# Optimization experiments

Hardware: AMD Instinct MI355X
Metric: run time of the kernel (lower is better)

Reference implementation:

```python
import jax, jax.numpy as jnp
import numpy as np

# ActivationWithGain: activation scaled so a standard-normal input keeps unit variance.
_s = np.random.default_rng(0).standard_normal(1 << 20).astype(np.float32)
GAIN = float(1.0 / (_s / (1.0 + np.exp(-_s))).std())  # SiLU gain ~ 1.787
INV_SQRT2 = np.float32(1.0 / np.sqrt(2.0))


def _act(x):
    return jax.nn.silu(x) * jnp.float32(GAIN)


def setup_inputs() -> dict:
    key = jax.random.key(0)
    ks = jax.random.split(key, 9)
    n_up, n_dn, n_nuc, dim, edim = 512, 512, 256, 256, 32
    n_el = n_up + n_dn
    n_edges = n_el * n_nuc  # dense electron-nucleus bipartite graph
    return {
        "elec_emb": jax.random.normal(ks[0], (n_el, dim), jnp.float32),
        "up_inp": jax.random.normal(ks[1], (n_nuc, dim), jnp.float32),
        "down_inp": jax.random.normal(ks[2], (n_nuc, dim), jnp.float32),
        "edge_emb": jax.random.normal(ks[3], (n_edges, edim), jnp.float32),
        "contr": jax.random.uniform(ks[4], (n_edges,), jnp.float32),
        "norm": jax.random.uniform(ks[5], (n_el,), jnp.float32),
        "W_out": jax.random.normal(ks[6], (dim, dim), jnp.float32) / np.float32(np.sqrt(dim)),
        "b_out": jnp.zeros((dim,), jnp.float32),
        "W_edge": jax.random.normal(ks[7], (edim, dim), jnp.float32) / np.float32(np.sqrt(edim)),
        "W_out2": jax.random.normal(ks[8], (dim, dim), jnp.float32) / np.float32(np.sqrt(dim)),
        "b_out2": jnp.zeros((dim,), jnp.float32),
        "scale1": jnp.ones((), jnp.float32),  # FixedScalingFactor (frozen after init)
        "scale2": jnp.ones((), jnp.float32),
        "n_up": n_up,
        "n_down": n_dn,
        "n_nuclei": n_nuc,
    }


def reference(elec_emb, up_inp, down_inp, edge_emb, contr, norm,
              W_out, b_out, W_edge, W_out2, b_out2, scale1, scale2,
              n_up, n_down, n_nuclei):
    n_el = n_up + n_down
    # adj_idx for a single graph: dense bipartite edges, sorted by electron index
    e_n_i = jnp.repeat(jnp.arange(n_el), n_nuclei)   # [E] electron index per edge
    e_n_k = jnp.tile(jnp.arange(n_nuclei), n_el)     # [E] nucleus index per edge

    out_emb = elec_emb @ W_out + b_out               # Dense(out_dim)

    mask = jnp.arange(n_el) < n_up                   # spin_mask: True for spin-up electrons
    e_n_mask = mask[e_n_i]
    # gather nuclear embeddings per edge, selecting up/down table by electron spin
    inp = jnp.where(e_n_mask[:, None], up_inp[e_n_k], down_inp[e_n_k])  # [E, D]

    weights = edge_emb @ W_edge                      # Dense_no_bias(out_dim), [E, D]
    # FixedScalingFactor: contr only weights the init-time variance estimate;
    # at runtime the op is x * scale1.
    to_elec = inp * weights * scale1                 # [E, D]

    agg = jax.ops.segment_sum(to_elec, e_n_i, num_segments=n_el,
                              indices_are_sorted=True)  # [n_el, D]
    out_emb = (out_emb + agg * norm[:, None]) * scale2
    out_emb = _act(out_emb)
    out_emb = _act(out_emb @ W_out2 + b_out2)
    # residual: shapes match, so rescaled sum
    return (elec_emb + out_emb) * INV_SQRT2
```

## Files before the change

kernel.cpp:

```cpp
#include <hip/hip_runtime.h>
#include <hip/hip_bf16.h>

#define N_EL   1024
#define N_UP   512
#define NNUC   256
#define DIM    256
#define EDIM   32

#define GAIN_F      1.7872135f
#define INV_SQRT2_F 0.7071067811865476f

typedef __attribute__((ext_vector_type(8))) short bf16x8;
typedef __attribute__((ext_vector_type(4))) short bf16x4;
typedef __attribute__((ext_vector_type(4))) float f32x4;

__device__ __forceinline__ short f2bf(float x) {
    union { __hip_bfloat16 h; short s; } u;
    u.h = __float2bfloat16(x);
    return u.s;
}

__global__ __launch_bounds__(256) void prep_kernel(
    const float* __restrict__ up, const float* __restrict__ dn,
    const float* __restrict__ wedge,
    const float* __restrict__ w1, const float* __restrict__ w2,
    const float* __restrict__ elec,
    float* __restrict__ tab_up, float* __restrict__ tab_dn,
    short* __restrict__ wedge_arr,
    short* __restrict__ w1f, short* __restrict__ w2f,
    short* __restrict__ elecb)
{
    const int idx = (blockIdx.x << 8) + threadIdx.x;

    {
        const int kt = idx >> 12;
        const int dt = (idx >> 8) & 15;
        const int l  = (idx >> 2) & 63;
        const int r  = idx & 3;
        const int row = (kt << 4) + ((l >> 4) << 2) + r;
        const int col = (dt << 4) + (l & 15);
        tab_up[idx] = up[row * DIM + col];
        tab_dn[idx] = dn[row * DIM + col];
    }
    if (idx < 16 * 64 * 8) {
        const int dt2 = idx >> 9;
        const int l2  = (idx >> 3) & 63;
        const int b   = idx & 7;
        const int j   = ((l2 >> 4) << 3) + b;
        const int d   = (dt2 << 4) + (l2 & 15);
        wedge_arr[idx] = f2bf(wedge[j * DIM + d]);
    }
    {
        const int b  = idx & 7;
        const int l  = (idx >> 3) & 63;
        const int q  = (idx >> 9) & 7;
        const int nt = idx >> 12;
        const int j  = (q << 5) + ((l >> 4) << 3) + b;
        const int d  = (nt << 4) + (l & 15);
        w1f[idx] = f2bf(w1[j * DIM + d]);
        w2f[idx] = f2bf(w2[j * DIM + d]);
    }
    {
        const f32x4 v = *(const f32x4*)(elec + (idx << 2));
        bf16x4 o;
        o[0] = f2bf(v[0]); o[1] = f2bf(v[1]); o[2] = f2bf(v[2]); o[3] = f2bf(v[3]);
        *(bf16x4*)(elecb + (idx << 2)) = o;
    }
}

__global__ __launch_bounds__(256) void fused_kernel(
    const float* __restrict__ eemb,
    const float* __restrict__ tab_up, const float* __restrict__ tab_dn,
    const short* __restrict__ wedge_arr,
    const short* __restrict__ w1f, const short* __restrict__ w2f,
    const short* __restrict__ elecb, const float* __restrict__ elec,
    const float* __restrict__ norm,
    const float* __restrict__ b1, const float* __restrict__ b2,
    const float* __restrict__ s1p, const float* __restrict__ s2p,
    float* __restrict__ outp)
{
    __shared__ float part[4][4][256];
    __shared__ float agg_s[4][256];
    __shared__ short h_s[4][256];

    const int tid  = threadIdx.x;
    const int bid  = blockIdx.x;
    const int w    = tid >> 6;
    const int lane = tid & 63;
    const int g    = lane >> 4;
    const int c    = lane & 15;
    const int base = bid << 2;

    {
        const float* __restrict__ tab = (base < N_UP) ? tab_up : tab_dn;

        bf16x8 a[4][4];
        #pragma unroll
        for (int e = 0; e < 4; ++e) {
            #pragma unroll
            for (int q = 0; q < 4; ++q) {
                const int kt = (w << 2) + q;
                const float* src = eemb +
                    ((size_t)((base + e) * NNUC + (kt << 4) + c) * EDIM + (g << 3));
                f32x4 lo = *(const f32x4*)(src);
                f32x4 hi = *(const f32x4*)(src + 4);
                union { bf16x8 v; short s[8]; } f;
                f.s[0] = f2bf(lo[0]); f.s[1] = f2bf(lo[1]);
                f.s[2] = f2bf(lo[2]); f.s[3] = f2bf(lo[3]);
                f.s[4] = f2bf(hi[0]); f.s[5] = f2bf(hi[1]);
                f.s[6] = f2bf(hi[2]); f.s[7] = f2bf(hi[3]);
                a[e][q] = f.v;
            }
        }

        const int kt0 = (w << 2);
        bf16x8 bnxt = *(const bf16x8*)(wedge_arr + (lane << 3));
        f32x4 tn0, tn1, tn2, tn3;
        tn0 = *(const f32x4*)(tab + ((((kt0 + 0) << 4) + 0) * 64 + lane) * 4);
        tn1 = *(const f32x4*)(tab + ((((kt0 + 1) << 4) + 0) * 64 + lane) * 4);
        tn2 = *(const f32x4*)(tab + ((((kt0 + 2) << 4) + 0) * 64 + lane) * 4);
        tn3 = *(const f32x4*)(tab + ((((kt0 + 3) << 4) + 0) * 64 + lane) * 4);

        const f32x4 zero4 = {0.f, 0.f, 0.f, 0.f};

        #pragma unroll 1
        for (int dt = 0; dt < 16; ++dt) {
            const bf16x8 bcur = bnxt;
            const f32x4 t0 = tn0, t1 = tn1, t2 = tn2, t3 = tn3;
            if (dt < 15) {
                bnxt = *(const bf16x8*)(wedge_arr + (((dt + 1) << 6) + lane) * 8);
                tn0 = *(const f32x4*)(tab + ((((kt0 + 0) << 4) + dt + 1) * 64 + lane) * 4);
                tn1 = *(const f32x4*)(tab + ((((kt0 + 1) << 4) + dt + 1) * 64 + lane) * 4);
                tn2 = *(const f32x4*)(tab + ((((kt0 + 2) << 4) + dt + 1) * 64 + lane) * 4);
                tn3 = *(const f32x4*)(tab + ((((kt0 + 3) << 4) + dt + 1) * 64 + lane) * 4);
            }
            float p[4] = {0.f, 0.f, 0.f, 0.f};
            #pragma unroll
            for (int e = 0; e < 4; ++e) {
                f32x4 cc;
                cc = __builtin_amdgcn_mfma_f32_16x16x32_bf16(a[e][0], bcur, zero4, 0, 0, 0);
                p[e] += cc[0] * t0[0] + cc[1] * t0[1] + cc[2] * t0[2] + cc[3] * t0[3];
                cc = __builtin_amdgcn_mfma_f32_16x16x32_bf16(a[e][1], bcur, zero4, 0, 0, 0);
                p[e] += cc[0] * t1[0] + cc[1] * t1[1] + cc[2] * t1[2] + cc[3] * t1[3];
                cc = __builtin_amdgcn_mfma_f32_16x16x32_bf16(a[e][2], bcur, zero4, 0, 0, 0);
                p[e] += cc[0] * t2[0] + cc[1] * t2[1] + cc[2] * t2[2] + cc[3] * t2[3];
                cc = __builtin_amdgcn_mfma_f32_16x16x32_bf16(a[e][3], bcur, zero4, 0, 0, 0);
                p[e] += cc[0] * t3[0] + cc[1] * t3[1] + cc[2] * t3[2] + cc[3] * t3[3];
            }
            #pragma unroll
            for (int e = 0; e < 4; ++e) {
                float v = p[e];
                v += __shfl_xor(v, 16, 64);
                v += __shfl_xor(v, 32, 64);
                if (lane < 16) part[w][e][(dt << 4) + lane] = v;
            }
        }
    }
    __syncthreads();
    {
        const float s1 = *s1p;
        for (int t = tid; t < 4 * 256; t += 256) {
            const int e = t >> 8;
            const int d = t & 255;
            agg_s[e][d] = (part[0][e][d] + part[1][e][d] +
                           part[2][e][d] + part[3][e][d]) * s1;
        }
    }
    __syncthreads();

    {
        const float s2 = *s2p;
        const int arow = (base + c) & (N_EL - 1);
        const short* abase = elecb + (arow << 8) + (g << 3);

        bf16x8 a[8];
        #pragma unroll
        for (int q = 0; q < 8; ++q) a[q] = *(const bf16x8*)(abase + (q << 5));

        const short* bb0 = w1f + ((w << 2) << 12) + (lane << 3);
        bf16x8 b[8], bn[8];
        #pragma unroll
        for (int q = 0; q < 8; ++q) bn[q] = *(const bf16x8*)(bb0 + (q << 9));

        #pragma unroll
        for (int t = 0; t < 4; ++t) {
            #pragma unroll
            for (int q = 0; q < 8; ++q) b[q] = bn[q];
            if (t < 3) {
                const short* bbn = bb0 + ((t + 1) << 12);
                #pragma unroll
                for (int q = 0; q < 8; ++q) bn[q] = *(const bf16x8*)(bbn + (q << 9));
            }
            f32x4 acc = {0.f, 0.f, 0.f, 0.f};
            #pragma unroll
            for (int q = 0; q < 8; ++q)
                acc = __builtin_amdgcn_mfma_f32_16x16x32_bf16(a[q], b[q], acc, 0, 0, 0);

            if (g == 0) {
                const int nt = (w << 2) + t;
                const int n  = (nt << 4) + c;
                const float bv = b1[n];
                #pragma unroll
                for (int r = 0; r < 4; ++r) {
                    const float y = (acc[r] + bv + agg_s[r][n] * norm[base + r]) * s2;
                    const float sig = 1.f / (1.f + __expf(-y));
                    h_s[r][n] = f2bf(GAIN_F * y * sig);
                }
            }
        }
    }
    __syncthreads();

    {
        bf16x8 a[8];
        #pragma unroll
        for (int q = 0; q < 8; ++q)
            a[q] = *(const bf16x8*)(&h_s[c & 3][(q << 5) + (g << 3)]);

        const short* bb0 = w2f + ((w << 2) << 12) + (lane << 3);
        bf16x8 b[8], bn[8];
        #pragma unroll
        for (int q = 0; q < 8; ++q) bn[q] = *(const bf16x8*)(bb0 + (q << 9));

        #pragma unroll
        for (int t = 0; t < 4; ++t) {
            #pragma unroll
            for (int q = 0; q < 8; ++q) b[q] = bn[q];
            if (t < 3) {
                const short* bbn = bb0 + ((t + 1) << 12);
                #pragma unroll
                for (int q = 0; q < 8; ++q) bn[q] = *(const bf16x8*)(bbn + (q << 9));
            }
            f32x4 acc = {0.f, 0.f, 0.f, 0.f};
            #pragma unroll
            for (int q = 0; q < 8; ++q)
                acc = __builtin_amdgcn_mfma_f32_16x16x32_bf16(a[q], b[q], acc, 0, 0, 0);

            if (g == 0) {
                const int nt = (w << 2) + t;
                const int n  = (nt << 4) + c;
                const float bv = b2[n];
                #pragma unroll
                for (int r = 0; r < 4; ++r) {
                    const float z = acc[r] + bv;
                    const float sig = 1.f / (1.f + __expf(-z));
                    const float o = GAIN_F * z * sig;
                    const int m = base + r;
                    outp[(m << 8) + n] = (elec[(m << 8) + n] + o) * INV_SQRT2_F;
                }
            }
        }
    }
}

extern "C" void kernel_launch(void* const* d_in, const int* in_sizes, int n_in,
                              void* d_out, int out_size, void* d_ws, size_t ws_size,
                              hipStream_t stream)
{
    const float* elec  = (const float*)d_in[0];
    const float* up    = (const float*)d_in[1];
    const float* dn    = (const float*)d_in[2];
    const float* eemb  = (const float*)d_in[3];
    const float* norm  = (const float*)d_in[5];
    const float* W1    = (const float*)d_in[6];
    const float* b1    = (const float*)d_in[7];
    const float* Wedge = (const float*)d_in[8];
    const float* W2    = (const float*)d_in[9];
    const float* b2    = (const float*)d_in[10];
    const float* s1    = (const float*)d_in[11];
    const float* s2    = (const float*)d_in[12];

    float* ws     = (float*)d_ws;
    float* tab_up = ws;
    float* tab_dn = ws + 65536;
    short* sbase  = (short*)(ws + 131072);
    short* warr   = sbase;
    short* w1f    = sbase + 8192;
    short* w2f    = sbase + 8192 + 65536;
    short* elecb  = sbase + 8192 + 131072;

    prep_kernel <<<256, 256, 0, stream>>>(up, dn, Wedge, W1, W2, elec,
                                          tab_up, tab_dn, warr, w1f, w2f, elecb);
    fused_kernel<<<256, 256, 0, stream>>>(eemb, tab_up, tab_dn, warr, w1f, w2f,
                                          elecb, elec, norm, b1, b2, s1, s2,
                                          (float*)d_out);
}
```

Baseline: 34.43 us.

## Split fused kernel into edge aggregation and separate 16-row output MLP kernel

Splits the single fused kernel into an edge kernel, which writes the aggregated per-electron vectors to a global workspace, and a separate output kernel. The output kernel runs both dense layers on 16-row tiles, so each MFMA uses all 16 rows. The old fused version padded 4 real rows to 16, which wasted most of the MFMA work and re-read the weight matrices in every one of 256 blocks. The cost is an extra kernel launch, a round trip through global memory for the aggregate, and only 64 blocks in the output stage.

After: 36.24 us. +5.3%, slower.

```diff
diff --git a/kernel.cpp b/kernel.cpp
--- a/kernel.cpp
+++ b/kernel.cpp
@@ -68,187 +68,171 @@
     }
 }
 
-__global__ __launch_bounds__(256) void fused_kernel(
+__global__ __launch_bounds__(256) void edge_kernel(
     const float* __restrict__ eemb,
     const float* __restrict__ tab_up, const float* __restrict__ tab_dn,
     const short* __restrict__ wedge_arr,
-    const short* __restrict__ w1f, const short* __restrict__ w2f,
-    const short* __restrict__ elecb, const float* __restrict__ elec,
-    const float* __restrict__ norm,
-    const float* __restrict__ b1, const float* __restrict__ b2,
-    const float* __restrict__ s1p, const float* __restrict__ s2p,
-    float* __restrict__ outp)
+    const float* __restrict__ s1p,
+    float* __restrict__ agg)
 {
     __shared__ float part[4][4][256];
-    __shared__ float agg_s[4][256];
-    __shared__ short h_s[4][256];
-
     const int tid  = threadIdx.x;
-    const int bid  = blockIdx.x;
     const int w    = tid >> 6;
     const int lane = tid & 63;
     const int g    = lane >> 4;
     const int c    = lane & 15;
-    const int base = bid << 2;
-
-    {
-        const float* __restrict__ tab = (base < N_UP) ? tab_up : tab_dn;
-
-        bf16x8 a[4][4];
+    const int base = blockIdx.x << 2;
+    const float* __restrict__ tab = (base < N_UP) ? tab_up : tab_dn;
+
+    bf16x8 a[4][4];
+    #pragma unroll
+    for (int e = 0; e < 4; ++e) {
+        #pragma unroll
+        for (int q = 0; q < 4; ++q) {
+            const int kt = (w << 2) + q;
+            const float* src = eemb +
+                ((size_t)((base + e) * NNUC + (kt << 4) + c) * EDIM + (g << 3));
+            f32x4 lo = *(const f32x4*)(src);
+            f32x4 hi = *(const f32x4*)(src + 4);
+            union { bf16x8 v; short s[8]; } f;
+            f.s[0] = f2bf(lo[0]); f.s[1] = f2bf(lo[1]);
+            f.s[2] = f2bf(lo[2]); f.s[3] = f2bf(lo[3]);
+            f.s[4] = f2bf(hi[0]); f.s[5] = f2bf(hi[1]);
+            f.s[6] = f2bf(hi[2]); f.s[7] = f2bf(hi[3]);
+            a[e][q] = f.v;
+        }
+    }
+
+    const int kt0 = (w << 2);
+    bf16x8 bnxt = *(const bf16x8*)(wedge_arr + (lane << 3));
+    f32x4 tn0, tn1, tn2, tn3;
+    tn0 = *(const f32x4*)(tab + ((((kt0 + 0) << 4) + 0) * 64 + lane) * 4);
+    tn1 = *(const f32x4*)(tab + ((((kt0 + 1) << 4) + 0) * 64 + lane) * 4);
+    tn2 = *(const f32x4*)(tab + ((((kt0 + 2) << 4) + 0) * 64 + lane) * 4);
+    tn3 = *(const f32x4*)(tab + ((((kt0 + 3) << 4) + 0) * 64 + lane) * 4);
+
+    const f32x4 zero4 = {0.f, 0.f, 0.f, 0.f};
+
+    #pragma unroll 1
+    for (int dt = 0; dt < 16; ++dt) {
+        const bf16x8 bcur = bnxt;
+        const f32x4 t0 = tn0, t1 = tn1, t2 = tn2, t3 = tn3;
+        if (dt < 15) {
+            bnxt = *(const bf16x8*)(wedge_arr + (((dt + 1) << 6) + lane) * 8);
+            tn0 = *(const f32x4*)(tab + ((((kt0 + 0) << 4) + dt + 1) * 64 + lane) * 4);
+            tn1 = *(const f32x4*)(tab + ((((kt0 + 1) << 4) + dt + 1) * 64 + lane) * 4);
+            tn2 = *(const f32x4*)(tab + ((((kt0 + 2) << 4) + dt + 1) * 64 + lane) * 4);
+            tn3 = *(const f32x4*)(tab + ((((kt0 + 3) << 4) + dt + 1) * 64 + lane) * 4);
+        }
+        float p[4] = {0.f, 0.f, 0.f, 0.f};
         #pragma unroll
         for (int e = 0; e < 4; ++e) {
-            #pragma unroll
-            for (int q = 0; q < 4; ++q) {
-                const int kt = (w << 2) + q;
-                const float* src = eemb +
-                    ((size_t)((base + e) * NNUC + (kt << 4) + c) * EDIM + (g << 3));
-                f32x4 lo = *(const f32x4*)(src);
-                f32x4 hi = *(const f32x4*)(src + 4);
-                union { bf16x8 v; short s[8]; } f;
-                f.s[0] = f2bf(lo[0]); f.s[1] = f2bf(lo[1]);
-                f.s[2] = f2bf(lo[2]); f.s[3] = f2bf(lo[3]);
-                f.s[4] = f2bf(hi[0]); f.s[5] = f2bf(hi[1]);
-                f.s[6] = f2bf(hi[2]); f.s[7] = f2bf(hi[3]);
-                a[e][q] = f.v;
-            }
-        }
-
-        const int kt0 = (w << 2);
-        bf16x8 bnxt = *(const bf16x8*)(wedge_arr + (lane << 3));
-        f32x4 tn0, tn1, tn2, tn3;
-        tn0 = *(const f32x4*)(tab + ((((kt0 + 0) << 4) + 0) * 64 + lane) * 4);
-        tn1 = *(const f32x4*)(tab + ((((kt0 + 1) << 4) + 0) * 64 + lane) * 4);
-        tn2 = *(const f32x4*)(tab + ((((kt0 + 2) << 4) + 0) * 64 + lane) * 4);
-        tn3 = *(const f32x4*)(tab + ((((kt0 + 3) << 4) + 0) * 64 + lane) * 4);
-
-        const f32x4 zero4 = {0.f, 0.f, 0.f, 0.f};
-
-        #pragma unroll 1
-        for (int dt = 0; dt < 16; ++dt) {
-            const bf16x8 bcur = bnxt;
-            const f32x4 t0 = tn0, t1 = tn1, t2 = tn2, t3 = tn3;
-            if (dt < 15) {
-                bnxt = *(const bf16x8*)(wedge_arr + (((dt + 1) << 6) + lane) * 8);
-                tn0 = *(const f32x4*)(tab + ((((kt0 + 0) << 4) + dt + 1) * 64 + lane) * 4);
-                tn1 = *(const f32x4*)(tab + ((((kt0 + 1) << 4) + dt + 1) * 64 + lane) * 4);
-                tn2 = *(const f32x4*)(tab + ((((kt0 + 2) << 4) + dt + 1) * 64 + lane) * 4);
-                tn3 = *(const f32x4*)(tab + ((((kt0 + 3) << 4) + dt + 1) * 64 + lane) * 4);
-            }
-            float p[4] = {0.f, 0.f, 0.f, 0.f};
-            #pragma unroll
-            for (int e = 0; e < 4; ++e) {
-                f32x4 cc;
-                cc = __builtin_amdgcn_mfma_f32_16x16x32_bf16(a[e][0], bcur, zero4, 0, 0, 0);
-                p[e] += cc[0] * t0[0] + cc[1] * t0[1] + cc[2] * t0[2] + cc[3] * t0[3];
-                cc = __builtin_amdgcn_mfma_f32_16x16x32_bf16(a[e][1], bcur, zero4, 0, 0, 0);
-                p[e] += cc[0] * t1[0] + cc[1] * t1[1] + cc[2] * t1[2] + cc[3] * t1[3];
-                cc = __builtin_amdgcn_mfma_f32_16x16x32_bf16(a[e][2], bcur, zero4, 0, 0, 0);
-                p[e] += cc[0] * t2[0] + cc[1] * t2[1] + cc[2] * t2[2] + cc[3] * t2[3];
-                cc = __builtin_amdgcn_mfma_f32_16x16x32_bf16(a[e][3], bcur, zero4, 0, 0, 0);
-                p[e] += cc[0] * t3[0] + cc[1] * t3[1] + cc[2] * t3[2] + cc[3] * t3[3];
-            }
-            #pragma unroll
-            for (int e = 0; e < 4; ++e) {
-                float v = p[e];
-                v += __shfl_xor(v, 16, 64);
-                v += __shfl_xor(v, 32, 64);
-                if (lane < 16) part[w][e][(dt << 4) + lane] = v;
-            }
+            f32x4 cc;
+            cc = __builtin_amdgcn_mfma_f32_16x16x32_bf16(a[e][0], bcur, zero4, 0, 0, 0);
+            p[e] += cc[0] * t0[0] + cc[1] * t0[1] + cc[2] * t0[2] + cc[3] * t0[3];
+            cc = __builtin_amdgcn_mfma_f32_16x16x32_bf16(a[e][1], bcur, zero4, 0, 0, 0);
+            p[e] += cc[0] * t1[0] + cc[1] * t1[1] + cc[2] * t1[2] + cc[3] * t1[3];
+            cc = __builtin_amdgcn_mfma_f32_16x16x32_bf16(a[e][2], bcur, zero4, 0, 0, 0);
+            p[e] += cc[0] * t2[0] + cc[1] * t2[1] + cc[2] * t2[2] + cc[3] * t2[3];
+            cc = __builtin_amdgcn_mfma_f32_16x16x32_bf16(a[e][3], bcur, zero4, 0, 0, 0);
+            p[e] += cc[0] * t3[0] + cc[1] * t3[1] + cc[2] * t3[2] + cc[3] * t3[3];
+        }
+        #pragma unroll
+        for (int e = 0; e < 4; ++e) {
+            float v = p[e];
+            v += __shfl_xor(v, 16, 64);
+            v += __shfl_xor(v, 32, 64);
+            if (lane < 16) part[w][e][(dt << 4) + lane] = v;
         }
     }
     __syncthreads();
-    {
-        const float s1 = *s1p;
-        for (int t = tid; t < 4 * 256; t += 256) {
-            const int e = t >> 8;
-            const int d = t & 255;
-            agg_s[e][d] = (part[0][e][d] + part[1][e][d] +
-                           part[2][e][d] + part[3][e][d]) * s1;
+
+    const float s1 = *s1p;
+    for (int t = tid; t < 4 * 256; t += 256) {
+        const int e = t >> 8;
+        const int d = t & 255;
+        const float s = part[0][e][d] + part[1][e][d] +
+                        part[2][e][d] + part[3][e][d];
+        agg[(size_t)(base + e) * DIM + d] = s * s1;
+    }
+}
+
+__global__ __launch_bounds__(512) void out_kernel(
+    const short* __restrict__ elecb,
+    const short* __restrict__ w1f, const short* __restrict__ w2f,
+    const float* __restrict__ elec, const float* __restrict__ agg,
+    const float* __restrict__ norm,
+    const float* __restrict__ b1, const float* __restrict__ b2,
+    const float* __restrict__ s2p,
+    float* __restrict__ outp)
+{
+    __shared__ short h_s[16][264];
+
+    const int tid  = threadIdx.x;
+    const int w    = tid >> 6;
+    const int lane = tid & 63;
+    const int g    = lane >> 4;
+    const int c    = lane & 15;
+    const int mb   = blockIdx.x << 4;
+
+    const short* abase = elecb + ((mb + c) << 8) + (g << 3);
+    bf16x8 a[8];
+    #pragma unroll
+    for (int q = 0; q < 8; ++q) a[q] = *(const bf16x8*)(abase + (q << 5));
+
+    const float s2 = *s2p;
+
+    #pragma unroll
+    for (int t = 0; t < 2; ++t) {
+        const int ct = (w << 1) + t;
+        const short* bb = w1f + (ct << 12) + (lane << 3);
+        bf16x8 b[8];
+        #pragma unroll
+        for (int q = 0; q < 8; ++q) b[q] = *(const bf16x8*)(bb + (q << 9));
+        f32x4 acc = {0.f, 0.f, 0.f, 0.f};
+        #pragma unroll
+        for (int q = 0; q < 8; ++q)
+            acc = __builtin_amdgcn_mfma_f32_16x16x32_bf16(a[q], b[q], acc, 0, 0, 0);
+
+        const int n  = (ct << 4) + c;
+        const float bv = b1[n];
+        #pragma unroll
+        for (int r = 0; r < 4; ++r) {
+            const int mr = (g << 2) + r;
+            const int m  = mb + mr;
+            const float y = (acc[r] + bv + agg[(m << 8) + n] * norm[m]) * s2;
+            const float sig = 1.f / (1.f + __expf(-y));
+            h_s[mr][n] = f2bf(GAIN_F * y * sig);
         }
     }
     __syncthreads();
 
-    {
-        const float s2 = *s2p;
-        const int arow = (base + c) & (N_EL - 1);
-        const short* abase = elecb + (arow << 8) + (g << 3);
-
-        bf16x8 a[8];
-        #pragma unroll
-        for (int q = 0; q < 8; ++q) a[q] = *(const bf16x8*)(abase + (q << 5));
-
-        const short* bb0 = w1f + ((w << 2) << 12) + (lane << 3);
-        bf16x8 b[8], bn[8];
-        #pragma unroll
-        for (int q = 0; q < 8; ++q) bn[q] = *(const bf16x8*)(bb0 + (q << 9));
-
-        #pragma unroll
-        for (int t = 0; t < 4; ++t) {
-            #pragma unroll
-            for (int q = 0; q < 8; ++q) b[q] = bn[q];
-            if (t < 3) {
-                const short* bbn = bb0 + ((t + 1) << 12);
-                #pragma unroll
-                for (int q = 0; q < 8; ++q) bn[q] = *(const bf16x8*)(bbn + (q << 9));
-            }
-            f32x4 acc = {0.f, 0.f, 0.f, 0.f};
-            #pragma unroll
-            for (int q = 0; q < 8; ++q)
-                acc = __builtin_amdgcn_mfma_f32_16x16x32_bf16(a[q], b[q], acc, 0, 0, 0);
-
-            if (g == 0) {
-                const int nt = (w << 2) + t;
-                const int n  = (nt << 4) + c;
-                const float bv = b1[n];
-                #pragma unroll
-                for (int r = 0; r < 4; ++r) {
-                    const float y = (acc[r] + bv + agg_s[r][n] * norm[base + r]) * s2;
-                    const float sig = 1.f / (1.f + __expf(-y));
-                    h_s[r][n] = f2bf(GAIN_F * y * sig);
-                }
-            }
-        }
-    }
-    __syncthreads();
-
-    {
-        bf16x8 a[8];
+    bf16x8 a2[8];
+    #pragma unroll
+    for (int q = 0; q < 8; ++q)
+        a2[q] = *(const bf16x8*)(&h_s[c][(q << 5) + (g << 3)]);
+
+    #pragma unroll
+    for (int t = 0; t < 2; ++t) {
+        const int ct = (w << 1) + t;
+        const short* bb = w2f + (ct << 12) + (lane << 3);
+        bf16x8 b[8];
+        #pragma unroll
+        for (int q = 0; q < 8; ++q) b[q] = *(const bf16x8*)(bb + (q << 9));
+        f32x4 acc = {0.f, 0.f, 0.f, 0.f};
         #pragma unroll
         for (int q = 0; q < 8; ++q)
-            a[q] = *(const bf16x8*)(&h_s[c & 3][(q << 5) + (g << 3)]);
-
-        const short* bb0 = w2f + ((w << 2) << 12) + (lane << 3);
-        bf16x8 b[8], bn[8];
-        #pragma unroll
-        for (int q = 0; q < 8; ++q) bn[q] = *(const bf16x8*)(bb0 + (q << 9));
-
-        #pragma unroll
-        for (int t = 0; t < 4; ++t) {
-            #pragma unroll
-            for (int q = 0; q < 8; ++q) b[q] = bn[q];
-            if (t < 3) {
-                const short* bbn = bb0 + ((t + 1) << 12);
-                #pragma unroll
-                for (int q = 0; q < 8; ++q) bn[q] = *(const bf16x8*)(bbn + (q << 9));
-            }
-            f32x4 acc = {0.f, 0.f, 0.f, 0.f};
-            #pragma unroll
-            for (int q = 0; q < 8; ++q)
-                acc = __builtin_amdgcn_mfma_f32_16x16x32_bf16(a[q], b[q], acc, 0, 0, 0);
-
-            if (g == 0) {
-                const int nt = (w << 2) + t;
-                const int n  = (nt << 4) + c;
-                const float bv = b2[n];
-                #pragma unroll
-                for (int r = 0; r < 4; ++r) {
-                    const float z = acc[r] + bv;
-                    const float sig = 1.f / (1.f + __expf(-z));
-                    const float o = GAIN_F * z * sig;
-                    const int m = base + r;
-                    outp[(m << 8) + n] = (elec[(m << 8) + n] + o) * INV_SQRT2_F;
-                }
-            }
+            acc = __builtin_amdgcn_mfma_f32_16x16x32_bf16(a2[q], b[q], acc, 0, 0, 0);
+
+        const int n  = (ct << 4) + c;
+        const float bv = b2[n];
+        #pragma unroll
+        for (int r = 0; r < 4; ++r) {
+            const int m = mb + (g << 2) + r;
+            const float z = acc[r] + bv;
+            const float sig = 1.f / (1.f + __expf(-z));
+            const float o = GAIN_F * z * sig;
+            outp[(m << 8) + n] = (elec[(m << 8) + n] + o) * INV_SQRT2_F;
         }
     }
 }
@@ -278,10 +262,11 @@
     short* w1f    = sbase + 8192;
     short* w2f    = sbase + 8192 + 65536;
     short* elecb  = sbase + 8192 + 131072;
-
-    prep_kernel <<<256, 256, 0, stream>>>(up, dn, Wedge, W1, W2, elec,
-                                          tab_up, tab_dn, warr, w1f, w2f, elecb);
-    fused_kernel<<<256, 256, 0, stream>>>(eemb, tab_up, tab_dn, warr, w1f, w2f,
-                                          elecb, elec, norm, b1, b2, s1, s2,
-                                          (float*)d_out);
-}
+    float* agg    = (float*)(sbase + 8192 + 131072 + 262144);
+
+    prep_kernel<<<256, 256, 0, stream>>>(up, dn, Wedge, W1, W2, elec,
+                                         tab_up, tab_dn, warr, w1f, w2f, elecb);
+    edge_kernel<<<256, 256, 0, stream>>>(eemb, tab_up, tab_dn, warr, s1, agg);
+    out_kernel <<<64, 512, 0, stream>>>(elecb, w1f, w2f, elec, agg, norm,
+                                        b1, b2, s2, (float*)d_out);
+}
```
